# Kernel optimization log

Hardware: AMD Instinct MI355X
Metric: run time of the kernel (lower is better)

Reference implementation:

```python
import jax, jax.numpy as jnp
import numpy as np
import math

D_SINGLE, D_PAIR, H, PQ, PV = 384, 128, 12, 4, 8
DH = D_SINGLE // H
OUT_DIM = H * DH + H * PV * 4 + H * D_PAIR


def setup_inputs() -> dict:
    key = jax.random.key(0)
    ks = jax.random.split(key, 24)
    B, L = 1, 512
    inp = {
        'single': jax.random.normal(ks[0], (B, L, D_SINGLE), jnp.float32),
        'pair': jax.random.normal(ks[1], (B, L, L, D_PAIR), jnp.float32),
        'rot_mats': jax.random.normal(ks[2], (B, L, 3, 3), jnp.float32),
        'trans': jax.random.normal(ks[3], (B, L, 3), jnp.float32),
        'mask': jnp.ones((B, L), jnp.float32),
        'ln_w': jnp.ones((D_SINGLE,), jnp.float32),
        'ln_b': jnp.zeros((D_SINGLE,), jnp.float32),
        'Wq': jax.random.normal(ks[4], (D_SINGLE, H * DH), jnp.float32) * 0.02,
        'bq': jnp.zeros((H * DH,), jnp.float32),
        'Wk': jax.random.normal(ks[5], (D_SINGLE, H * DH), jnp.float32) * 0.02,
        'bk': jnp.zeros((H * DH,), jnp.float32),
        'Wv': jax.random.normal(ks[6], (D_SINGLE, H * DH), jnp.float32) * 0.02,
        'bv': jnp.zeros((H * DH,), jnp.float32),
        'Wqp': jax.random.normal(ks[7], (D_SINGLE, H * PQ * 3), jnp.float32) * 0.02,
        'bqp': jnp.zeros((H * PQ * 3,), jnp.float32),
        'Wkp': jax.random.normal(ks[8], (D_SINGLE, H * PQ * 3), jnp.float32) * 0.02,
        'bkp': jnp.zeros((H * PQ * 3,), jnp.float32),
        'Wvp': jax.random.normal(ks[9], (D_SINGLE, H * PV * 3), jnp.float32) * 0.02,
        'bvp': jnp.zeros((H * PV * 3,), jnp.float32),
        'Wpb': jax.random.normal(ks[10], (D_PAIR, H), jnp.float32) * 0.02,
        'bpb': jnp.zeros((H,), jnp.float32),
        'Wo': jax.random.normal(ks[11], (OUT_DIM, D_SINGLE), jnp.float32) * 0.02,
        'bo': jnp.zeros((D_SINGLE,), jnp.float32),
        'w_c': jnp.asarray(1.0 / math.sqrt(3.0), jnp.float32),
        'w_l': jnp.asarray(1.0 / 3.0, jnp.float32),
        'gamma_h': jnp.ones((H,), jnp.float32),
    }
    return inp


def _layer_norm(x, w, b, eps=1e-5):
    mu = jnp.mean(x, axis=-1, keepdims=True)
    var = jnp.mean((x - mu) ** 2, axis=-1, keepdims=True)
    return (x - mu) * jax.lax.rsqrt(var + eps) * w + b


def reference(single, pair, rot_mats, trans, mask, ln_w, ln_b, Wq, bq, Wk, bk, Wv, bv,
              Wqp, bqp, Wkp, bkp, Wvp, bvp, Wpb, bpb, Wo, bo, w_c, w_l, gamma_h):
    B, L, _ = single.shape
    sn = _layer_norm(single, ln_w, ln_b)
    q = (sn @ Wq + bq).reshape(B, L, H, DH)
    k = (sn @ Wk + bk).reshape(B, L, H, DH)
    v = (sn @ Wv + bv).reshape(B, L, H, DH)
    qp = (sn @ Wqp + bqp).reshape(B, L, H, PQ, 3)
    kp = (sn @ Wkp + bkp).reshape(B, L, H, PQ, 3)
    vp = (sn @ Wvp + bvp).reshape(B, L, H, PV, 3)

    t = trans[:, :, None, None, :]  # [B,L,1,1,3]
    qg = jnp.einsum('blij,blhpj->blhpi', rot_mats, qp) + t
    kg = jnp.einsum('blij,blhpj->blhpi', rot_mats, kp) + t
    vg = jnp.einsum('blij,blhpj->blhpi', rot_mats, vp) + t

    # sequence logits [B,H,L,L]
    seq_logits = jnp.einsum('bihd,bjhd->bhij', q, k) * w_c / math.sqrt(DH)

    # geometric logits: pairwise point distances [B,H,L,L]
    q_pts = jnp.transpose(qg, (0, 2, 1, 3, 4))  # [B,H,L,PQ,3]
    k_pts = jnp.transpose(kg, (0, 2, 1, 3, 4))
    diff = q_pts[:, :, :, None] - k_pts[:, :, None]  # [B,H,L,L,PQ,3]
    dist_sq = jnp.sum(diff ** 2, axis=-1)            # [B,H,L,L,PQ]
    geo_logits = -0.5 * jnp.sum(dist_sq, axis=-1) * gamma_h[None, :, None, None] * w_l

    pair_bias = jnp.transpose(pair @ Wpb + bpb, (0, 3, 1, 2))  # [B,H,L,L]
    logits = seq_logits + geo_logits + pair_bias

    mask_2d = (mask[:, :, None] * mask[:, None, :])[:, None]  # [B,1,L,L]
    logits = jnp.where(mask_2d > 0, logits, jnp.float32(-1e9))
    attn = jax.nn.softmax(logits, axis=-1)  # [B,H,L,L]

    # sequence aggregation -> [B,L,H,DH]
    seq_out = jnp.einsum('bhij,bjhd->bihd', attn, v).reshape(B, L, H * DH)

    # point aggregation -> local frame features
    pts_out = jnp.einsum('bhij,bjhpd->bihpd', attn, vg)  # [B,L,H,PV,3]
    pts_local = jnp.einsum('blji,blhpj->blhpi', rot_mats, pts_out - t)
    pts_norm = jnp.linalg.norm(pts_local, axis=-1, keepdims=True)
    pts_feat = jnp.concatenate([pts_norm, pts_local], axis=-1).reshape(B, L, H * PV * 4)

    # pair aggregation -> [B,L,H*D_PAIR]
    pair_out = jnp.einsum('bhij,bijd->bihd', attn, pair).reshape(B, L, H * D_PAIR)

    combined = jnp.concatenate([seq_out, pts_feat, pair_out], axis=-1)
    return combined @ Wo + bo
```

## Files before the change

kernel.cpp:

```cpp
#include <hip/hip_runtime.h>
#include <math.h>

#define LQ   512
#define DS   384
#define DPAIR 128
#define NH   12
#define NPP  1792
#define FE   48
#define TJ   128

__global__ void k_concat_w(const float* __restrict__ Wq, const float* __restrict__ Wk,
                           const float* __restrict__ Wv, const float* __restrict__ Wqp,
                           const float* __restrict__ Wkp, const float* __restrict__ Wvp,
                           const float* __restrict__ bq, const float* __restrict__ bk,
                           const float* __restrict__ bv, const float* __restrict__ bqp,
                           const float* __restrict__ bkp, const float* __restrict__ bvp,
                           float* __restrict__ Wcat, float* __restrict__ bcat) {
  int idx = blockIdx.x * 256 + threadIdx.x;
  const int total = DS * NPP;
  if (idx < total) {
    int k = idx / NPP, c = idx % NPP;
    float v = 0.f;
    if (c < 384)       v = Wq[k*384 + c];
    else if (c < 768)  v = Wk[k*384 + c-384];
    else if (c < 1152) v = Wv[k*384 + c-768];
    else if (c < 1296) v = Wqp[k*144 + c-1152];
    else if (c < 1440) v = Wkp[k*144 + c-1296];
    else if (c < 1728) v = Wvp[k*288 + c-1440];
    Wcat[idx] = v;
  } else if (idx < total + NPP) {
    int c = idx - total;
    float v = 0.f;
    if (c < 384)       v = bq[c];
    else if (c < 768)  v = bk[c-384];
    else if (c < 1152) v = bv[c-768];
    else if (c < 1296) v = bqp[c-1152];
    else if (c < 1440) v = bkp[c-1296];
    else if (c < 1728) v = bvp[c-1440];
    bcat[c] = v;
  }
}

__global__ void k_wpbt(const float* __restrict__ Wpb, float* __restrict__ WpbT) {
  int e = blockIdx.x * 256 + threadIdx.x;
  if (e >= DPAIR * NH) return;
  int k = e / NH, h = e % NH;
  WpbT[h*DPAIR + k] = Wpb[e];
}

__global__ __launch_bounds__(128) void k_layernorm(const float* __restrict__ x,
                                                   const float* __restrict__ w,
                                                   const float* __restrict__ b,
                                                   float* __restrict__ y) {
  __shared__ float red[128];
  __shared__ float s_mu, s_rstd;
  int i = blockIdx.x, t = threadIdx.x;
  float v0 = x[i*DS + t], v1 = x[i*DS + t + 128], v2 = x[i*DS + t + 256];
  red[t] = v0 + v1 + v2; __syncthreads();
  for (int s = 64; s > 0; s >>= 1) { if (t < s) red[t] += red[t+s]; __syncthreads(); }
  if (t == 0) s_mu = red[0] * (1.f/384.f);
  __syncthreads();
  float mu = s_mu;
  float d0 = v0-mu, d1 = v1-mu, d2 = v2-mu;
  red[t] = d0*d0 + d1*d1 + d2*d2; __syncthreads();
  for (int s = 64; s > 0; s >>= 1) { if (t < s) red[t] += red[t+s]; __syncthreads(); }
  if (t == 0) s_rstd = rsqrtf(red[0] * (1.f/384.f) + 1e-5f);
  __syncthreads();
  float r = s_rstd;
  y[i*DS + t      ] = d0*r*w[t      ] + b[t      ];
  y[i*DS + t + 128] = d1*r*w[t + 128] + b[t + 128];
  y[i*DS + t + 256] = d2*r*w[t + 256] + b[t + 256];
}

__global__ __launch_bounds__(256) void k_gemm_nn(const float* __restrict__ A,
                                                 const float* __restrict__ B,
                                                 const float* __restrict__ bias,
                                                 float* __restrict__ C,
                                                 float* __restrict__ Cpart,
                                                 int M, int N, int K) {
  __shared__ float As[16*68];
  __shared__ float Bs[16*68];
  int t = threadIdx.x;
  int mg = t >> 4, ng = t & 15;
  int i0 = blockIdx.y * 64, j0 = blockIdx.x * 64;
  int KS = gridDim.z;
  int kper = K / KS;
  int kbeg = blockIdx.z * kper;
  float acc[4][4] = {};
  for (int k0 = kbeg; k0 < kbeg + kper; k0 += 16) {
    int e = t;
    #pragma unroll
    for (int s = 0; s < 4; s++, e += 256) {
      int m = e >> 4, k = e & 15;
      As[k*68 + m] = A[(size_t)(i0+m)*K + k0 + k];
      int k2 = e >> 6, n = e & 63;
      Bs[k2*68 + n] = B[(size_t)(k0+k2)*N + j0 + n];
    }
    __syncthreads();
    #pragma unroll
    for (int k = 0; k < 16; k++) {
      float4 av = *(const float4*)(As + k*68 + mg*4);
      float4 bv = *(const float4*)(Bs + k*68 + ng*4);
      float a[4] = {av.x, av.y, av.z, av.w};
      float b[4] = {bv.x, bv.y, bv.z, bv.w};
      #pragma unroll
      for (int y = 0; y < 4; y++)
        #pragma unroll
        for (int x = 0; x < 4; x++)
          acc[y][x] = fmaf(a[y], b[x], acc[y][x]);
    }
    __syncthreads();
  }
  if (KS == 1) {
    #pragma unroll
    for (int y = 0; y < 4; y++) {
      int m = i0 + mg*4 + y;
      #pragma unroll
      for (int x = 0; x < 4; x++) {
        int n = j0 + ng*4 + x;
        C[(size_t)m*N + n] = acc[y][x] + bias[n];
      }
    }
  } else {
    float* dst = Cpart + (size_t)blockIdx.z * M * N;
    #pragma unroll
    for (int y = 0; y < 4; y++) {
      int m = i0 + mg*4 + y;
      #pragma unroll
      for (int x = 0; x < 4; x++) {
        int n = j0 + ng*4 + x;
        dst[(size_t)m*N + n] = acc[y][x];
      }
    }
  }
}

__global__ void k_reduce_bias(const float* __restrict__ part, const float* __restrict__ bias,
                              float* __restrict__ out, int MN, int N, int KS) {
  int e = blockIdx.x * 256 + threadIdx.x;
  if (e >= MN) return;
  float s = bias[e % N];
  for (int z = 0; z < KS; z++) s += part[(size_t)z*MN + e];
  out[e] = s;
}

__global__ void k_rotate(const float* __restrict__ C1, const float* __restrict__ rot,
                         const float* __restrict__ trans, float* __restrict__ qg,
                         float* __restrict__ kg, float* __restrict__ vg) {
  int idx = blockIdx.x * 256 + threadIdx.x;
  if (idx >= LQ*NH*16) return;
  int w = idx & 15; int h = (idx >> 4) % NH; int i = idx / (16*NH);
  const float* R = rot + (size_t)i*9;
  const float* tr = trans + (size_t)i*3;
  const float* src; float* dst;
  if (w < 4)      { src = C1 + (size_t)i*NPP + 1152 + h*12 + w*3;     dst = qg + ((size_t)i*NH + h)*12 + w*3; }
  else if (w < 8) { int p = w-4; src = C1 + (size_t)i*NPP + 1296 + h*12 + p*3; dst = kg + ((size_t)i*NH + h)*12 + p*3; }
  else            { int p = w-8; src = C1 + (size_t)i*NPP + 1440 + h*24 + p*3; dst = vg + ((size_t)i*NH + h)*24 + p*3; }
  float x = src[0], y = src[1], z = src[2];
  dst[0] = fmaf(R[0],x, fmaf(R[1],y, fmaf(R[2],z, tr[0])));
  dst[1] = fmaf(R[3],x, fmaf(R[4],y, fmaf(R[5],z, tr[1])));
  dst[2] = fmaf(R[6],x, fmaf(R[7],y, fmaf(R[8],z, tr[2])));
}

__global__ void k_features(const float* __restrict__ C1, const float* __restrict__ qg,
                           const float* __restrict__ kg, const float* __restrict__ gamma,
                           const float* __restrict__ w_c, const float* __restrict__ w_l,
                           float* __restrict__ Af, float* __restrict__ Bf) {
  int idx = blockIdx.x * 256 + threadIdx.x;
  if (idx >= LQ*NH) return;
  int h = idx % NH, i = idx / NH;
  float s  = w_c[0] * rsqrtf(32.f);
  float gp = gamma[h] * w_l[0];
  float* a  = Af + ((size_t)h*LQ + i)*FE;
  float* bb = Bf + ((size_t)h*LQ + i)*FE;
  const float* q = C1 + (size_t)i*NPP + h*32;
  const float* k = C1 + (size_t)i*NPP + 384 + h*32;
  for (int d = 0; d < 32; d++) { a[d] = s*q[d]; bb[d] = k[d]; }
  const float* qp = qg + ((size_t)i*NH + h)*12;
  const float* kp = kg + ((size_t)i*NH + h)*12;
  float sq = 0.f, sk = 0.f;
  for (int d = 0; d < 12; d++) {
    float x = qp[d], y = kp[d];
    a[32+d] = gp*x; bb[32+d] = y;
    sq = fmaf(x,x,sq); sk = fmaf(y,y,sk);
  }
  a[44] = -0.5f*gp*sq; a[45] = 1.f; a[46] = 0.f; a[47] = 0.f;
  bb[44] = 1.f; bb[45] = -0.5f*gp*sk; bb[46] = 0.f; bb[47] = 0.f;
}

__global__ __launch_bounds__(256) void k_logits_nt(const float* __restrict__ Af,
                                                   const float* __restrict__ Bf,
                                                   float* __restrict__ S) {
  __shared__ float As[48*68];
  __shared__ float Bs[48*68];
  int h = blockIdx.z;
  int i0 = blockIdx.y * 64, j0 = blockIdx.x * 64;
  int t = threadIdx.x;
  int mg = t >> 4, ng = t & 15;
  const float* Ah = Af + (size_t)h*LQ*FE;
  const float* Bh = Bf + (size_t)h*LQ*FE;
  for (int e = t; e < 64*48; e += 256) {
    int m = e / 48, k = e % 48;
    As[k*68 + m] = Ah[(size_t)(i0+m)*FE + k];
    Bs[k*68 + m] = Bh[(size_t)(j0+m)*FE + k];
  }
  __syncthreads();
  float acc[4][4] = {};
  #pragma unroll 8
  for (int k = 0; k < 48; k++) {
    float4 av = *(const float4*)(As + k*68 + mg*4);
    float4 bv = *(const float4*)(Bs + k*68 + ng*4);
    float a[4] = {av.x, av.y, av.z, av.w};
    float b[4] = {bv.x, bv.y, bv.z, bv.w};
    #pragma unroll
    for (int y = 0; y < 4; y++)
      #pragma unroll
      for (int x = 0; x < 4; x++)
        acc[y][x] = fmaf(a[y], b[x], acc[y][x]);
  }
  #pragma unroll
  for (int y = 0; y < 4; y++) {
    #pragma unroll
    for (int x = 0; x < 4; x++)
      S[((size_t)h*LQ + i0 + mg*4 + y)*LQ + j0 + ng*4 + x] = acc[y][x];
  }
}

__global__ __launch_bounds__(512, 2) void k_pair_fused(
    const float* __restrict__ pair, const float* __restrict__ WpbT,
    const float* __restrict__ bpb, const float* __restrict__ mask,
    float* __restrict__ S, float* __restrict__ comb) {
  __shared__ float tile[TJ*133];
  __shared__ float logit[NH*LQ];
  __shared__ float wt[NH*TJ];
  __shared__ float m_s[NH], s_s[NH], alpha_s[NH];
  int i = blockIdx.x, t = threadIdx.x;
  float mi = mask[i];

  for (int e = t; e < NH*LQ; e += 512) {
    int h = e >> 9, j = e & 511;
    logit[e] = S[((size_t)h*LQ + i)*LQ + j] + bpb[h];
  }
  if (t < NH) { m_s[t] = -3.0e38f; s_s[t] = 0.f; alpha_s[t] = 0.f; }

  const float* psrc = pair + (size_t)i*LQ*DPAIR;
  float4 r[8];
  #pragma unroll
  for (int u = 0; u < 8; u++) r[u] = ((const float4*)psrc)[t + u*512];

  float4 acc[NH];
  #pragma unroll
  for (int h = 0; h < NH; h++) acc[h] = make_float4(0.f,0.f,0.f,0.f);

  for (int jt = 0; jt < LQ/TJ; jt++) {
    #pragma unroll
    for (int u = 0; u < 8; u++) {
      int e = t + u*512; int row = e >> 5, c4 = e & 31;
      *(float4*)&tile[row*133 + c4*4] = r[u];
    }
    __syncthreads();
    if (jt < LQ/TJ - 1) {
      const float4* nsrc = (const float4*)(psrc + (size_t)(jt+1)*TJ*DPAIR);
      #pragma unroll
      for (int u = 0; u < 8; u++) r[u] = nsrc[t + u*512];
    }

    {
      int j = t & 127;
      int hg = __builtin_amdgcn_readfirstlane(t >> 7);
      const float* w0p = WpbT + (hg*3+0)*DPAIR;
      const float* w1p = WpbT + (hg*3+1)*DPAIR;
      const float* w2p = WpbT + (hg*3+2)*DPAIR;
      float a0 = 0.f, a1 = 0.f, a2 = 0.f;
      #pragma unroll 8
      for (int k = 0; k < DPAIR; k += 4) {
        float4 pv = *(const float4*)&tile[j*133 + k];
        float4 w0 = *(const float4*)(w0p + k);
        float4 w1 = *(const float4*)(w1p + k);
        float4 w2 = *(const float4*)(w2p + k);
        a0 = fmaf(pv.x,w0.x, fmaf(pv.y,w0.y, fmaf(pv.z,w0.z, fmaf(pv.w,w0.w, a0))));
        a1 = fmaf(pv.x,w1.x, fmaf(pv.y,w1.y, fmaf(pv.z,w1.z, fmaf(pv.w,w1.w, a1))));
        a2 = fmaf(pv.x,w2.x, fmaf(pv.y,w2.y, fmaf(pv.z,w2.z, fmaf(pv.w,w2.w, a2))));
      }
      int jj = jt*TJ + j;
      bool dead = (mi * mask[jj] <= 0.f);
      int h0 = hg*3;
      float l0 = logit[(h0+0)*LQ + jj] + a0;
      float l1 = logit[(h0+1)*LQ + jj] + a1;
      float l2 = logit[(h0+2)*LQ + jj] + a2;
      if (dead) { l0 = -1e9f; l1 = -1e9f; l2 = -1e9f; }
      logit[(h0+0)*LQ + jj] = l0;
      logit[(h0+1)*LQ + jj] = l1;
      logit[(h0+2)*LQ + jj] = l2;
    }
    __syncthreads();

    float lv[4];
    int sh = t >> 5, sl = t & 31;
    if (t < NH*32) {
      float mx = -3.0e38f;
      #pragma unroll
      for (int q = 0; q < 4; q++) {
        lv[q] = logit[sh*LQ + jt*TJ + sl + q*32];
        mx = fmaxf(mx, lv[q]);
      }
      #pragma unroll
      for (int o = 16; o > 0; o >>= 1) mx = fmaxf(mx, __shfl_xor(mx, o));
      if (sl == 0) {
        float mo = m_s[sh];
        float mn = fmaxf(mo, mx);
        alpha_s[sh] = __expf(mo - mn);
        m_s[sh] = mn;
      }
    }
    __syncthreads();
    if (t < NH*32) {
      float mn = m_s[sh];
      float sm = 0.f;
      #pragma unroll
      for (int q = 0; q < 4; q++) {
        float w = __expf(lv[q] - mn);
        wt[sh*TJ + sl + q*32] = w;
        sm += w;
      }
      #pragma unroll
      for (int o = 16; o > 0; o >>= 1) sm += __shfl_xor(sm, o);
      if (sl == 0) s_s[sh] = s_s[sh]*alpha_s[sh] + sm;
    }
    __syncthreads();

    {
      int dg = t & 31, strip = t >> 5;
      int jb = strip*8;
      float4 pv[8];
      #pragma unroll
      for (int q = 0; q < 8; q++) pv[q] = *(const float4*)&tile[(jb+q)*133 + dg*4];
      #pragma unroll
      for (int h = 0; h < NH; h++) {
        float al = alpha_s[h];
        float4 w0 = *(const float4*)&wt[h*TJ + jb];
        float4 w1 = *(const float4*)&wt[h*TJ + jb + 4];
        float wq[8] = {w0.x,w0.y,w0.z,w0.w,w1.x,w1.y,w1.z,w1.w};
        float4 a = acc[h];
        a.x *= al; a.y *= al; a.z *= al; a.w *= al;
        #pragma unroll
        for (int q = 0; q < 8; q++) {
          a.x = fmaf(wq[q], pv[q].x, a.x);
          a.y = fmaf(wq[q], pv[q].y, a.y);
          a.z = fmaf(wq[q], pv[q].z, a.z);
          a.w = fmaf(wq[q], pv[q].w, a.w);
        }
        acc[h] = a;
      }
    }
    __syncthreads();
  }

  for (int e = t; e < NH*LQ; e += 512) {
    int h = e >> 9, j = e & 511;
    float a = __expf(logit[e] - m_s[h]) / s_s[h];
    S[((size_t)h*LQ + i)*LQ + j] = a;
  }

  float4* red4 = (float4*)tile;
  int dg = t & 31, strip = t >> 5;
  float4 tot = make_float4(0.f,0.f,0.f,0.f);
  #pragma unroll
  for (int half = 0; half < 2; half++) {
    if ((strip >> 3) == half) {
      #pragma unroll
      for (int h = 0; h < NH; h++) red4[((strip & 7)*NH + h)*32 + dg] = acc[h];
    }
    __syncthreads();
    if (t < NH*32) {
      int h = t >> 5, d = t & 31;
      #pragma unroll
      for (int s8 = 0; s8 < 8; s8++) {
        float4 v = red4[(s8*NH + h)*32 + d];
        tot.x += v.x; tot.y += v.y; tot.z += v.z; tot.w += v.w;
      }
    }
    __syncthreads();
  }
  if (t < NH*32) {
    int h = t >> 5, d = t & 31;
    float is = 1.f / s_s[h];
    float4 o = make_float4(tot.x*is, tot.y*is, tot.z*is, tot.w*is);
    *(float4*)&comb[(size_t)i*2304 + 768 + h*DPAIR + d*4] = o;
  }
}

__global__ __launch_bounds__(256) void k_attn_v(const float* __restrict__ attn,
                                                const float* __restrict__ C1,
                                                const float* __restrict__ vg,
                                                float* __restrict__ psum) {
  __shared__ float As[64*68];
  __shared__ float Vs[64*68];
  int i0 = blockIdx.x * 64;
  int h = blockIdx.y;
  int z = blockIdx.z;
  int t = threadIdx.x;
  int mg = t >> 4, ng = t & 15;
  float acc[4][4] = {};
  for (int k0 = z*128; k0 < z*128 + 128; k0 += 64) {
    __syncthreads();
    for (int e = t; e < 64*64; e += 256) {
      int m = e >> 6, j = e & 63;
      As[j*68 + m] = attn[((size_t)h*LQ + i0 + m)*LQ + k0 + j];
    }
    for (int e = t; e < 64*64; e += 256) {
      int j = e >> 6, c = e & 63;
      float v = 0.f;
      if (c < 32)      v = C1[(size_t)(k0+j)*NPP + 768 + h*32 + c];
      else if (c < 56) v = vg[((size_t)(k0+j)*NH + h)*24 + (c-32)];
      Vs[j*68 + c] = v;
    }
    __syncthreads();
    #pragma unroll 4
    for (int j = 0; j < 64; j++) {
      float4 av = *(const float4*)(As + j*68 + mg*4);
      float4 bv = *(const float4*)(Vs + j*68 + ng*4);
      float a[4] = {av.x, av.y, av.z, av.w};
      float b[4] = {bv.x, bv.y, bv.z, bv.w};
      #pragma unroll
      for (int y = 0; y < 4; y++)
        #pragma unroll
        for (int x = 0; x < 4; x++)
          acc[y][x] = fmaf(a[y], b[x], acc[y][x]);
    }
  }
  #pragma unroll
  for (int y = 0; y < 4; y++) {
    int i = i0 + mg*4 + y;
    #pragma unroll
    for (int x = 0; x < 4; x++) {
      int n = ng*4 + x;
      psum[(((size_t)z*LQ + i)*NH + h)*64 + n] = acc[y][x];
    }
  }
}

__global__ void k_av_reduce(const float* __restrict__ psum, float* __restrict__ comb,
                            float* __restrict__ pts) {
  int e = blockIdx.x * 256 + threadIdx.x;
  if (e >= LQ*NH*56) return;
  int n = e % 56; int ih = e / 56; int h = ih % NH; int i = ih / NH;
  size_t base = ((size_t)i*NH + h)*64 + n;
  float s = 0.f;
  for (int z = 0; z < 4; z++) s += psum[(size_t)z*LQ*NH*64 + base];
  if (n < 32) comb[(size_t)i*2304 + h*32 + n] = s;
  else        pts[((size_t)i*NH + h)*24 + (n-32)] = s;
}

__global__ void k_pts_feat(const float* __restrict__ pts, const float* __restrict__ rot,
                           const float* __restrict__ trans, float* __restrict__ comb) {
  int idx = blockIdx.x * 256 + threadIdx.x;
  if (idx >= LQ*NH*8) return;
  int p = idx & 7; int h = (idx >> 3) % NH; int i = idx / (8*NH);
  const float* R = rot + (size_t)i*9;
  const float* tr = trans + (size_t)i*3;
  const float* pt = pts + ((size_t)i*NH + h)*24 + p*3;
  float x = pt[0]-tr[0], y = pt[1]-tr[1], z = pt[2]-tr[2];
  float lx = fmaf(R[0],x, fmaf(R[3],y, R[6]*z));
  float ly = fmaf(R[1],x, fmaf(R[4],y, R[7]*z));
  float lz = fmaf(R[2],x, fmaf(R[5],y, R[8]*z));
  float nrm = sqrtf(fmaf(lx,lx, fmaf(ly,ly, lz*lz)));
  float* dst = comb + (size_t)i*2304 + 384 + (h*8 + p)*4;
  dst[0] = nrm; dst[1] = lx; dst[2] = ly; dst[3] = lz;
}

extern "C" void kernel_launch(void* const* d_in, const int* in_sizes, int n_in,
                              void* d_out, int out_size, void* d_ws, size_t ws_size,
                              hipStream_t stream) {
  const float* single = (const float*)d_in[0];
  const float* pair   = (const float*)d_in[1];
  const float* rot    = (const float*)d_in[2];
  const float* trans  = (const float*)d_in[3];
  const float* mask   = (const float*)d_in[4];
  const float* ln_w   = (const float*)d_in[5];
  const float* ln_b   = (const float*)d_in[6];
  const float* Wq     = (const float*)d_in[7];
  const float* bq     = (const float*)d_in[8];
  const float* Wk     = (const float*)d_in[9];
  const float* bk     = (const float*)d_in[10];
  const float* Wv     = (const float*)d_in[11];
  const float* bv     = (const float*)d_in[12];
  const float* Wqp    = (const float*)d_in[13];
  const float* bqp    = (const float*)d_in[14];
  const float* Wkp    = (const float*)d_in[15];
  const float* bkp    = (const float*)d_in[16];
  const float* Wvp    = (const float*)d_in[17];
  const float* bvp    = (const float*)d_in[18];
  const float* Wpb    = (const float*)d_in[19];
  const float* bpb    = (const float*)d_in[20];
  const float* Wo     = (const float*)d_in[21];
  const float* bo     = (const float*)d_in[22];
  const float* w_c    = (const float*)d_in[23];
  const float* w_l    = (const float*)d_in[24];
  const float* gamma  = (const float*)d_in[25];
  float* out = (float*)d_out;

  float* p = (float*)d_ws;
  auto alloc = [&](size_t n) { float* r = p; p += n; return r; };
  float* Wcat   = alloc((size_t)DS*NPP);
  float* bcat   = alloc(NPP);
  float* WpbT   = alloc((size_t)NH*DPAIR);
  float* sn     = alloc((size_t)LQ*DS);
  float* C1     = alloc((size_t)LQ*NPP);
  float* qg     = alloc((size_t)LQ*NH*12);
  float* kg     = alloc((size_t)LQ*NH*12);
  float* vgb    = alloc((size_t)LQ*NH*24);
  float* Af     = alloc((size_t)NH*LQ*FE);
  float* Bf     = alloc((size_t)NH*LQ*FE);
  float* S      = alloc((size_t)NH*LQ*LQ);
  float* comb   = alloc((size_t)LQ*2304);
  float* pts    = alloc((size_t)LQ*NH*24);
  float* scratch= alloc((size_t)8*LQ*DS);

  k_concat_w<<<dim3((DS*NPP + NPP + 255)/256), 256, 0, stream>>>(
      Wq, Wk, Wv, Wqp, Wkp, Wvp, bq, bk, bv, bqp, bkp, bvp, Wcat, bcat);
  k_wpbt<<<dim3((DPAIR*NH + 255)/256), 256, 0, stream>>>(Wpb, WpbT);
  k_layernorm<<<dim3(LQ), 128, 0, stream>>>(single, ln_w, ln_b, sn);
  k_gemm_nn<<<dim3(NPP/64, LQ/64, 1), 256, 0, stream>>>(sn, Wcat, bcat, C1, nullptr, LQ, NPP, DS);
  k_rotate<<<dim3((LQ*NH*16 + 255)/256), 256, 0, stream>>>(C1, rot, trans, qg, kg, vgb);
  k_features<<<dim3((LQ*NH + 255)/256), 256, 0, stream>>>(C1, qg, kg, gamma, w_c, w_l, Af, Bf);
  k_logits_nt<<<dim3(LQ/64, LQ/64, NH), 256, 0, stream>>>(Af, Bf, S);
  k_pair_fused<<<dim3(LQ), 512, 0, stream>>>(pair, WpbT, bpb, mask, S, comb);
  k_attn_v<<<dim3(LQ/64, NH, 4), 256, 0, stream>>>(S, C1, vgb, scratch);
  k_av_reduce<<<dim3((LQ*NH*56 + 255)/256), 256, 0, stream>>>(scratch, comb, pts);
  k_pts_feat<<<dim3((LQ*NH*8 + 255)/256), 256, 0, stream>>>(pts, rot, trans, comb);
  k_gemm_nn<<<dim3(DS/64, LQ/64, 8), 256, 0, stream>>>(comb, Wo, bo, nullptr, scratch, LQ, DS, 2304);
  k_reduce_bias<<<dim3((LQ*DS + 255)/256), 256, 0, stream>>>(scratch, bo, out, LQ*DS, DS, 8);
}
```

Measured before the change: 418.0 us.

## Split fused pair-attention kernel into j-chunked blocks with split-softmax merge

Replaces the per-row fused pair-bias/softmax/pair-aggregation kernel (512 blocks looping over four j-tiles) with a 2D grid of 512x8 blocks, each handling a 64-wide j chunk with a local softmax. A separate merge kernel combines the per-chunk max/sum statistics, rescales the partial pair aggregates and rewrites the attention probabilities in S. The aim is more parallelism and occupancy with smaller blocks and no serial online-softmax loop. In exchange it adds an extra launch, extra global traffic for partial results, and a second read-modify-write pass over S.

New measurement: 386.6 us. -7.5%, faster.

```diff
diff --git a/kernel.cpp b/kernel.cpp
--- a/kernel.cpp
+++ b/kernel.cpp
@@ -1,13 +1,14 @@
 #include <hip/hip_runtime.h>
 #include <math.h>
 
-#define LQ   512
-#define DS   384
+#define LQ    512
+#define DS    384
 #define DPAIR 128
-#define NH   12
-#define NPP  1792
-#define FE   48
-#define TJ   128
+#define NH    12
+#define NPP   1792
+#define FE    48
+#define TJC   64
+#define NC    8
 
 __global__ void k_concat_w(const float* __restrict__ Wq, const float* __restrict__ Wk,
                            const float* __restrict__ Wv, const float* __restrict__ Wqp,
@@ -226,167 +227,159 @@
   }
 }
 
-__global__ __launch_bounds__(512, 2) void k_pair_fused(
+__global__ __launch_bounds__(256, 4) void k_pair_chunk(
     const float* __restrict__ pair, const float* __restrict__ WpbT,
     const float* __restrict__ bpb, const float* __restrict__ mask,
+    float* __restrict__ S, float* __restrict__ pairpart, float* __restrict__ msum) {
+  __shared__ float tile[TJC*133];
+  __shared__ float wt[NH*TJC];
+  int i = blockIdx.x, c = blockIdx.y, t = threadIdx.x;
+  int j0 = c*TJC;
+
+  const float4* src = (const float4*)(pair + ((size_t)i*LQ + j0)*DPAIR);
+  #pragma unroll
+  for (int u = 0; u < 8; u++) {
+    int e = t + u*256; int row = e >> 5, c4 = e & 31;
+    *(float4*)&tile[row*133 + c4*4] = src[e];
+  }
+
+  int j = t & 63;
+  int hg = __builtin_amdgcn_readfirstlane(t >> 6);
+  int h0 = hg*3;
+  float l[3];
+  #pragma unroll
+  for (int q = 0; q < 3; q++)
+    l[q] = S[((size_t)(h0+q)*LQ + i)*LQ + j0 + j] + bpb[h0+q];
+  bool dead = (mask[i] * mask[j0 + j] <= 0.f);
+  __syncthreads();
+
+  {
+    const float* w0p = WpbT + (size_t)(h0+0)*DPAIR;
+    const float* w1p = WpbT + (size_t)(h0+1)*DPAIR;
+    const float* w2p = WpbT + (size_t)(h0+2)*DPAIR;
+    float a0 = 0.f, a1 = 0.f, a2 = 0.f;
+    #pragma unroll 8
+    for (int k = 0; k < DPAIR; k += 4) {
+      float4 pv = *(const float4*)&tile[j*133 + k];
+      float4 w0 = *(const float4*)(w0p + k);
+      float4 w1 = *(const float4*)(w1p + k);
+      float4 w2 = *(const float4*)(w2p + k);
+      a0 = fmaf(pv.x,w0.x, fmaf(pv.y,w0.y, fmaf(pv.z,w0.z, fmaf(pv.w,w0.w, a0))));
+      a1 = fmaf(pv.x,w1.x, fmaf(pv.y,w1.y, fmaf(pv.z,w1.z, fmaf(pv.w,w1.w, a1))));
+      a2 = fmaf(pv.x,w2.x, fmaf(pv.y,w2.y, fmaf(pv.z,w2.z, fmaf(pv.w,w2.w, a2))));
+    }
+    l[0] += a0; l[1] += a1; l[2] += a2;
+    if (dead) { l[0] = -1e9f; l[1] = -1e9f; l[2] = -1e9f; }
+  }
+
+  #pragma unroll
+  for (int q = 0; q < 3; q++) {
+    float m = l[q];
+    #pragma unroll
+    for (int o = 32; o > 0; o >>= 1) m = fmaxf(m, __shfl_xor(m, o, 64));
+    float w = __expf(l[q] - m);
+    float sm = w;
+    #pragma unroll
+    for (int o = 32; o > 0; o >>= 1) sm += __shfl_xor(sm, o, 64);
+    wt[(h0+q)*TJC + j] = w;
+    S[((size_t)(h0+q)*LQ + i)*LQ + j0 + j] = w;
+    if (j == 0) {
+      float* dst = msum + (((size_t)i*NC + c)*NH + h0 + q)*2;
+      dst[0] = m; dst[1] = sm;
+    }
+  }
+  __syncthreads();
+
+  int dg = t & 31, strip = t >> 5, jb = strip*8;
+  float4 pv[8];
+  #pragma unroll
+  for (int q = 0; q < 8; q++) pv[q] = *(const float4*)&tile[(jb+q)*133 + dg*4];
+  float4 acc[NH];
+  #pragma unroll
+  for (int h = 0; h < NH; h++) acc[h] = make_float4(0.f,0.f,0.f,0.f);
+  #pragma unroll
+  for (int h = 0; h < NH; h++) {
+    float4 w0 = *(const float4*)&wt[h*TJC + jb];
+    float4 w1 = *(const float4*)&wt[h*TJC + jb + 4];
+    float wq[8] = {w0.x,w0.y,w0.z,w0.w,w1.x,w1.y,w1.z,w1.w};
+    float4 a = acc[h];
+    #pragma unroll
+    for (int q = 0; q < 8; q++) {
+      a.x = fmaf(wq[q], pv[q].x, a.x);
+      a.y = fmaf(wq[q], pv[q].y, a.y);
+      a.z = fmaf(wq[q], pv[q].z, a.z);
+      a.w = fmaf(wq[q], pv[q].w, a.w);
+    }
+    acc[h] = a;
+  }
+  __syncthreads();
+
+  float4* red4 = (float4*)tile;
+  float4 tot[2];
+  tot[0] = make_float4(0.f,0.f,0.f,0.f);
+  tot[1] = make_float4(0.f,0.f,0.f,0.f);
+  #pragma unroll
+  for (int half = 0; half < 2; half++) {
+    if ((strip >> 2) == half) {
+      #pragma unroll
+      for (int h = 0; h < NH; h++)
+        red4[(((strip & 3)*NH) + h)*32 + dg] = acc[h];
+    }
+    __syncthreads();
+    for (int e = t, u = 0; e < NH*32; e += 256, u++) {
+      int rh = e >> 5, rd = e & 31;
+      #pragma unroll
+      for (int s4 = 0; s4 < 4; s4++) {
+        float4 v = red4[((s4*NH) + rh)*32 + rd];
+        tot[u].x += v.x; tot[u].y += v.y; tot[u].z += v.z; tot[u].w += v.w;
+      }
+    }
+    __syncthreads();
+  }
+  for (int e = t, u = 0; e < NH*32; e += 256, u++) {
+    int rh = e >> 5, rd = e & 31;
+    *(float4*)&pairpart[(((size_t)i*NC + c)*NH + rh)*DPAIR + rd*4] = tot[u];
+  }
+}
+
+__global__ __launch_bounds__(512) void k_merge(
+    const float* __restrict__ msum, const float* __restrict__ pairpart,
     float* __restrict__ S, float* __restrict__ comb) {
-  __shared__ float tile[TJ*133];
-  __shared__ float logit[NH*LQ];
-  __shared__ float wt[NH*TJ];
-  __shared__ float m_s[NH], s_s[NH], alpha_s[NH];
+  __shared__ float scs[NH*NC];
   int i = blockIdx.x, t = threadIdx.x;
-  float mi = mask[i];
-
+  if (t < NH) {
+    float m = -3.0e38f;
+    float mc[NC], sc_[NC];
+    #pragma unroll
+    for (int c = 0; c < NC; c++) {
+      const float* p = msum + (((size_t)i*NC + c)*NH + t)*2;
+      mc[c] = p[0]; sc_[c] = p[1];
+      m = fmaxf(m, mc[c]);
+    }
+    float s = 0.f;
+    #pragma unroll
+    for (int c = 0; c < NC; c++) s += sc_[c] * __expf(mc[c] - m);
+    float inv = 1.f / s;
+    #pragma unroll
+    for (int c = 0; c < NC; c++) scs[t*NC + c] = __expf(mc[c] - m) * inv;
+  }
+  __syncthreads();
+  if (t < NH*32) {
+    int h = t >> 5, d = t & 31;
+    float4 tot = make_float4(0.f,0.f,0.f,0.f);
+    #pragma unroll
+    for (int c = 0; c < NC; c++) {
+      float sc = scs[h*NC + c];
+      float4 v = *(const float4*)&pairpart[(((size_t)i*NC + c)*NH + h)*DPAIR + d*4];
+      tot.x = fmaf(v.x, sc, tot.x); tot.y = fmaf(v.y, sc, tot.y);
+      tot.z = fmaf(v.z, sc, tot.z); tot.w = fmaf(v.w, sc, tot.w);
+    }
+    *(float4*)&comb[(size_t)i*2304 + 768 + h*DPAIR + d*4] = tot;
+  }
   for (int e = t; e < NH*LQ; e += 512) {
     int h = e >> 9, j = e & 511;
-    logit[e] = S[((size_t)h*LQ + i)*LQ + j] + bpb[h];
-  }
-  if (t < NH) { m_s[t] = -3.0e38f; s_s[t] = 0.f; alpha_s[t] = 0.f; }
-
-  const float* psrc = pair + (size_t)i*LQ*DPAIR;
-  float4 r[8];
-  #pragma unroll
-  for (int u = 0; u < 8; u++) r[u] = ((const float4*)psrc)[t + u*512];
-
-  float4 acc[NH];
-  #pragma unroll
-  for (int h = 0; h < NH; h++) acc[h] = make_float4(0.f,0.f,0.f,0.f);
-
-  for (int jt = 0; jt < LQ/TJ; jt++) {
-    #pragma unroll
-    for (int u = 0; u < 8; u++) {
-      int e = t + u*512; int row = e >> 5, c4 = e & 31;
-      *(float4*)&tile[row*133 + c4*4] = r[u];
-    }
-    __syncthreads();
-    if (jt < LQ/TJ - 1) {
-      const float4* nsrc = (const float4*)(psrc + (size_t)(jt+1)*TJ*DPAIR);
-      #pragma unroll
-      for (int u = 0; u < 8; u++) r[u] = nsrc[t + u*512];
-    }
-
-    {
-      int j = t & 127;
-      int hg = __builtin_amdgcn_readfirstlane(t >> 7);
-      const float* w0p = WpbT + (hg*3+0)*DPAIR;
-      const float* w1p = WpbT + (hg*3+1)*DPAIR;
-      const float* w2p = WpbT + (hg*3+2)*DPAIR;
-      float a0 = 0.f, a1 = 0.f, a2 = 0.f;
-      #pragma unroll 8
-      for (int k = 0; k < DPAIR; k += 4) {
-        float4 pv = *(const float4*)&tile[j*133 + k];
-        float4 w0 = *(const float4*)(w0p + k);
-        float4 w1 = *(const float4*)(w1p + k);
-        float4 w2 = *(const float4*)(w2p + k);
-        a0 = fmaf(pv.x,w0.x, fmaf(pv.y,w0.y, fmaf(pv.z,w0.z, fmaf(pv.w,w0.w, a0))));
-        a1 = fmaf(pv.x,w1.x, fmaf(pv.y,w1.y, fmaf(pv.z,w1.z, fmaf(pv.w,w1.w, a1))));
-        a2 = fmaf(pv.x,w2.x, fmaf(pv.y,w2.y, fmaf(pv.z,w2.z, fmaf(pv.w,w2.w, a2))));
-      }
-      int jj = jt*TJ + j;
-      bool dead = (mi * mask[jj] <= 0.f);
-      int h0 = hg*3;
-      float l0 = logit[(h0+0)*LQ + jj] + a0;
-      float l1 = logit[(h0+1)*LQ + jj] + a1;
-      float l2 = logit[(h0+2)*LQ + jj] + a2;
-      if (dead) { l0 = -1e9f; l1 = -1e9f; l2 = -1e9f; }
-      logit[(h0+0)*LQ + jj] = l0;
-      logit[(h0+1)*LQ + jj] = l1;
-      logit[(h0+2)*LQ + jj] = l2;
-    }
-    __syncthreads();
-
-    float lv[4];
-    int sh = t >> 5, sl = t & 31;
-    if (t < NH*32) {
-      float mx = -3.0e38f;
-      #pragma unroll
-      for (int q = 0; q < 4; q++) {
-        lv[q] = logit[sh*LQ + jt*TJ + sl + q*32];
-        mx = fmaxf(mx, lv[q]);
-      }
-      #pragma unroll
-      for (int o = 16; o > 0; o >>= 1) mx = fmaxf(mx, __shfl_xor(mx, o));
-      if (sl == 0) {
-        float mo = m_s[sh];
-        float mn = fmaxf(mo, mx);
-        alpha_s[sh] = __expf(mo - mn);
-        m_s[sh] = mn;
-      }
-    }
-    __syncthreads();
-    if (t < NH*32) {
-      float mn = m_s[sh];
-      float sm = 0.f;
-      #pragma unroll
-      for (int q = 0; q < 4; q++) {
-        float w = __expf(lv[q] - mn);
-        wt[sh*TJ + sl + q*32] = w;
-        sm += w;
-      }
-      #pragma unroll
-      for (int o = 16; o > 0; o >>= 1) sm += __shfl_xor(sm, o);
-      if (sl == 0) s_s[sh] = s_s[sh]*alpha_s[sh] + sm;
-    }
-    __syncthreads();
-
-    {
-      int dg = t & 31, strip = t >> 5;
-      int jb = strip*8;
-      float4 pv[8];
-      #pragma unroll
-      for (int q = 0; q < 8; q++) pv[q] = *(const float4*)&tile[(jb+q)*133 + dg*4];
-      #pragma unroll
-      for (int h = 0; h < NH; h++) {
-        float al = alpha_s[h];
-        float4 w0 = *(const float4*)&wt[h*TJ + jb];
-        float4 w1 = *(const float4*)&wt[h*TJ + jb + 4];
-        float wq[8] = {w0.x,w0.y,w0.z,w0.w,w1.x,w1.y,w1.z,w1.w};
-        float4 a = acc[h];
-        a.x *= al; a.y *= al; a.z *= al; a.w *= al;
-        #pragma unroll
-        for (int q = 0; q < 8; q++) {
-          a.x = fmaf(wq[q], pv[q].x, a.x);
-          a.y = fmaf(wq[q], pv[q].y, a.y);
-          a.z = fmaf(wq[q], pv[q].z, a.z);
-          a.w = fmaf(wq[q], pv[q].w, a.w);
-        }
-        acc[h] = a;
-      }
-    }
-    __syncthreads();
-  }
-
-  for (int e = t; e < NH*LQ; e += 512) {
-    int h = e >> 9, j = e & 511;
-    float a = __expf(logit[e] - m_s[h]) / s_s[h];
-    S[((size_t)h*LQ + i)*LQ + j] = a;
-  }
-
-  float4* red4 = (float4*)tile;
-  int dg = t & 31, strip = t >> 5;
-  float4 tot = make_float4(0.f,0.f,0.f,0.f);
-  #pragma unroll
-  for (int half = 0; half < 2; half++) {
-    if ((strip >> 3) == half) {
-      #pragma unroll
-      for (int h = 0; h < NH; h++) red4[((strip & 7)*NH + h)*32 + dg] = acc[h];
-    }
-    __syncthreads();
-    if (t < NH*32) {
-      int h = t >> 5, d = t & 31;
-      #pragma unroll
-      for (int s8 = 0; s8 < 8; s8++) {
-        float4 v = red4[(s8*NH + h)*32 + d];
-        tot.x += v.x; tot.y += v.y; tot.z += v.z; tot.w += v.w;
-      }
-    }
-    __syncthreads();
-  }
-  if (t < NH*32) {
-    int h = t >> 5, d = t & 31;
-    float is = 1.f / s_s[h];
-    float4 o = make_float4(tot.x*is, tot.y*is, tot.z*is, tot.w*is);
-    *(float4*)&comb[(size_t)i*2304 + 768 + h*DPAIR + d*4] = o;
+    size_t idx = ((size_t)h*LQ + i)*LQ + j;
+    S[idx] *= scs[h*NC + (j >> 6)];
   }
 }
 
@@ -502,20 +495,22 @@
 
   float* p = (float*)d_ws;
   auto alloc = [&](size_t n) { float* r = p; p += n; return r; };
-  float* Wcat   = alloc((size_t)DS*NPP);
-  float* bcat   = alloc(NPP);
-  float* WpbT   = alloc((size_t)NH*DPAIR);
-  float* sn     = alloc((size_t)LQ*DS);
-  float* C1     = alloc((size_t)LQ*NPP);
-  float* qg     = alloc((size_t)LQ*NH*12);
-  float* kg     = alloc((size_t)LQ*NH*12);
-  float* vgb    = alloc((size_t)LQ*NH*24);
-  float* Af     = alloc((size_t)NH*LQ*FE);
-  float* Bf     = alloc((size_t)NH*LQ*FE);
-  float* S      = alloc((size_t)NH*LQ*LQ);
-  float* comb   = alloc((size_t)LQ*2304);
-  float* pts    = alloc((size_t)LQ*NH*24);
-  float* scratch= alloc((size_t)8*LQ*DS);
+  float* Wcat    = alloc((size_t)DS*NPP);
+  float* bcat    = alloc(NPP);
+  float* WpbT    = alloc((size_t)NH*DPAIR);
+  float* sn      = alloc((size_t)LQ*DS);
+  float* C1      = alloc((size_t)LQ*NPP);
+  float* qg      = alloc((size_t)LQ*NH*12);
+  float* kg      = alloc((size_t)LQ*NH*12);
+  float* vgb     = alloc((size_t)LQ*NH*24);
+  float* Af      = alloc((size_t)NH*LQ*FE);
+  float* Bf      = alloc((size_t)NH*LQ*FE);
+  float* S       = alloc((size_t)NH*LQ*LQ);
+  float* pairpart= alloc((size_t)LQ*NC*NH*DPAIR);
+  float* msum    = alloc((size_t)LQ*NC*NH*2);
+  float* comb    = alloc((size_t)LQ*2304);
+  float* pts     = alloc((size_t)LQ*NH*24);
+  float* scratch = alloc((size_t)8*LQ*DS);
 
   k_concat_w<<<dim3((DS*NPP + NPP + 255)/256), 256, 0, stream>>>(
       Wq, Wk, Wv, Wqp, Wkp, Wvp, bq, bk, bv, bqp, bkp, bvp, Wcat, bcat);
@@ -525,7 +520,8 @@
   k_rotate<<<dim3((LQ*NH*16 + 255)/256), 256, 0, stream>>>(C1, rot, trans, qg, kg, vgb);
   k_features<<<dim3((LQ*NH + 255)/256), 256, 0, stream>>>(C1, qg, kg, gamma, w_c, w_l, Af, Bf);
   k_logits_nt<<<dim3(LQ/64, LQ/64, NH), 256, 0, stream>>>(Af, Bf, S);
-  k_pair_fused<<<dim3(LQ), 512, 0, stream>>>(pair, WpbT, bpb, mask, S, comb);
+  k_pair_chunk<<<dim3(LQ, NC), 256, 0, stream>>>(pair, WpbT, bpb, mask, S, pairpart, msum);
+  k_merge<<<dim3(LQ), 512, 0, stream>>>(msum, pairpart, S, comb);
   k_attn_v<<<dim3(LQ/64, NH, 4), 256, 0, stream>>>(S, C1, vgb, scratch);
   k_av_reduce<<<dim3((LQ*NH*56 + 255)/256), 256, 0, stream>>>(scratch, comb, pts);
   k_pts_feat<<<dim3((LQ*NH*8 + 255)/256), 256, 0, stream>>>(pts, rot, trans, comb);
```
